# Optimization experiments

Hardware: AMD Instinct MI355X
Metric: run time of the kernel (lower is better)

Reference implementation:

```python
import jax, jax.numpy as jnp
import numpy as np

B, L, D, H = 32, 512, 512, 8          # batch(=num_nodes), seq len, model_size, num_heads
HD = D // H                            # head size
E_DIM, N_EDGES, N_PATHS = 128, 4096, 1024  # edge_dim (hardcoded 128), edge table, #(src,dst) pairs
MAXD = H                               # max_path_distance == num_heads


def setup_inputs() -> dict:
    rng = jax.random.key(0)
    ks = jax.random.split(rng, 16)
    n = lambda k, s: jax.random.normal(k, s, jnp.float32)
    idx = jnp.arange(N_PATHS)
    inp = {
        'query': n(ks[0], (B, L, D)),
        'key':   n(ks[1], (B, L, D)),
        'value': n(ks[2], (B, L, D)),
        'mask':  jnp.ones((B, 1, 1, L), jnp.float32),
        'edge_attr': n(ks[3], (N_EDGES, E_DIM)),
        'path_src': (idx // B).astype(jnp.int32),   # all (src,dst) node pairs
        'path_dst': (idx % B).astype(jnp.int32),
        'path_edges': jax.random.randint(ks[4], (N_PATHS, MAXD), 0, N_EDGES),
        'path_lens': jax.random.randint(ks[5], (N_PATHS,), 1, MAXD + 1),
        # learned params
        'WQ': n(ks[6], (D, D)) * 0.02, 'bQ': jnp.zeros((D,), jnp.float32),
        'WK': n(ks[7], (D, D)) * 0.02, 'bK': jnp.zeros((D,), jnp.float32),
        'WV': n(ks[8], (D, D)) * 0.02, 'bV': jnp.zeros((D,), jnp.float32),
        'WO': n(ks[9], (D, D)) * 0.02, 'bO': jnp.zeros((D,), jnp.float32),
        'edge_vector': n(ks[10], (MAXD, E_DIM)) * 0.05,  # EdgeEncoding weight
        'b_vec': n(ks[11], (MAXD,)) * 0.05,              # SpatialEncoding weight
        'b_scale': jnp.float32(0.001),
        'c_scale': jnp.float32(0.001),
    }
    return inp


def reference(query, key, value, mask, edge_attr, path_src, path_dst, path_edges,
              path_lens, WQ, bQ, WK, bK, WV, bV, WO, bO, edge_vector, b_vec,
              b_scale, c_scale):
    def split_heads(x):  # [B,L,D] -> [B,H,L,HD]
        return x.reshape(B, L, H, HD).transpose(0, 2, 1, 3)

    q = split_heads(jnp.einsum('bld,de->ble', query, WQ) + bQ)
    k = split_heads(jnp.einsum('bld,de->ble', key, WK) + bK)
    v = split_heads(jnp.einsum('bld,de->ble', value, WV) + bV)

    score = jnp.einsum('bhqd,bhkd->bhqk', q, k) / jnp.sqrt(jnp.float32(HD))

    pl = jnp.minimum(path_lens, MAXD).astype(jnp.int32)  # clipped path lengths

    # SpatialEncoding: spatial[src,dst] = b_vec[min(len,maxd)-1]
    spatial = jnp.zeros((B, B), jnp.float32).at[path_src, path_dst].set(b_vec[pl - 1])
    b_mean = spatial.mean(axis=1)  # [B]

    # EdgeEncoding: cij[src,dst] = mean_k <edge_vector[k], edge_attr[path[k]]>
    pe = edge_attr[path_edges]                       # [P,MAXD,E]  batched gather
    dots = jnp.einsum('ke,pke->pk', edge_vector, pe)  # [P,MAXD]
    kmask = (jnp.arange(MAXD)[None, :] < pl[:, None]).astype(jnp.float32)
    cvals = jnp.where(pl > 0, (dots * kmask).sum(1) / jnp.maximum(pl, 1), 0.0)
    cij = jnp.zeros((B, B), jnp.float32).at[path_src, path_dst].set(cvals)
    c_mean = cij.mean(axis=1)  # [B]

    bias = (b_scale * b_mean + c_scale * c_mean)[:, None, None, None]
    score = score + bias + (1.0 - mask) * (-1e9)

    alpha = jax.nn.softmax(score, axis=-1)
    ctx = jnp.einsum('bhqk,bhkd->bhqd', alpha, v)
    ctx = ctx.transpose(0, 2, 1, 3).reshape(B, L, D)
    return jnp.einsum('bld,de->ble', ctx, WO) + bO
```

## Files before the change

kernel.cpp:

```cpp
#include <hip/hip_runtime.h>
#include <hip/hip_bf16.h>

#define B_  32
#define L_  512
#define D_  512
#define H_  8
#define HD_ 64

typedef __attribute__((ext_vector_type(8))) short bf16x8;
typedef __attribute__((ext_vector_type(4))) short bf16x4;
typedef __attribute__((ext_vector_type(4))) float f32x4;

__device__ __forceinline__ short f2bf(float f) {
  union { float f; unsigned u; } x; x.f = f;
  unsigned r = x.u + 0x7FFFu + ((x.u >> 16) & 1u);
  return (short)(r >> 16);
}

__device__ __forceinline__ void gll16(const void* g, void* l) {
  __builtin_amdgcn_global_load_lds(
      (const __attribute__((address_space(1))) unsigned int*)g,
      (__attribute__((address_space(3))) unsigned int*)l, 16, 0, 0);
}

__device__ __forceinline__ bf16x8 cvt8(f32x4 a, f32x4 b) {
  union { __hip_bfloat162 h[4]; bf16x8 v; } u;
  u.h[0] = __float22bfloat162_rn(float2{a[0], a[1]});
  u.h[1] = __float22bfloat162_rn(float2{a[2], a[3]});
  u.h[2] = __float22bfloat162_rn(float2{b[0], b[1]});
  u.h[3] = __float22bfloat162_rn(float2{b[2], b[3]});
  return u.v;
}

#define DS_FENCE() do { asm volatile("s_waitcnt lgkmcnt(0)" ::: "memory"); \
                        __builtin_amdgcn_sched_barrier(0); } while (0)

__global__ __launch_bounds__(256) void wt_kernel(
    const float* __restrict__ WQ, const float* __restrict__ WK,
    const float* __restrict__ WV, const float* __restrict__ WO,
    short* __restrict__ wt) {
  __shared__ float tile[32][33];
  int wz = blockIdx.z;
  const float* W = (wz == 0) ? WQ : (wz == 1) ? WK : (wz == 2) ? WV : WO;
  int k0 = blockIdx.y * 32, n0 = blockIdx.x * 32;
  int tr = threadIdx.x >> 5, tc = threadIdx.x & 31;
#pragma unroll
  for (int i = 0; i < 4; ++i)
    tile[tr + i * 8][tc] = W[(size_t)(k0 + tr + i * 8) * D_ + n0 + tc];
  __syncthreads();
#pragma unroll
  for (int i = 0; i < 4; ++i)
    wt[((size_t)wz * D_ + n0 + tr + i * 8) * D_ + k0 + tc] =
        f2bf(tile[tc][tr + i * 8]);
}

__global__ __launch_bounds__(256, 3) void gemm_qkv(
    const float* __restrict__ Xq, const float* __restrict__ Xk,
    const float* __restrict__ Xv, const short* __restrict__ wt,
    const float* __restrict__ bQ, const float* __restrict__ bK,
    const float* __restrict__ bV,
    short* __restrict__ q_ws, short* __restrict__ k_ws,
    short* __restrict__ vt_ws) {
  __shared__ __align__(16) char lds[49152];
  char* Al = lds;
  char* Bl = lds + 16384;

  int mode = blockIdx.z;
  const float* A = (mode == 0) ? Xq : (mode == 1) ? Xk : Xv;
  const short* WT = wt + (size_t)mode * D_ * D_;
  const float* bias = (mode == 0) ? bQ : (mode == 1) ? bK : bV;

  int wgid = blockIdx.x + 2 * blockIdx.y;
  int xcd = wgid & 7, idx = wgid >> 3;
  int m0 = (xcd * 32 + (idx >> 1)) * 64;
  int n0 = (idx & 1) * 256;

  int tid = threadIdx.x, lane = tid & 63, w = tid >> 6;
  int wr = w >> 1, wc = w & 1, g = lane >> 4, lr = lane & 15;

  f32x4 acc[2][8] = {};

#pragma unroll
  for (int ks = 0; ks < 8; ++ks) {
    __syncthreads();
#pragma unroll
    for (int j = 0; j < 4; ++j) {
      int e = w * 4 + j;
      int row = e * 4 + (lane >> 4);
      int chunk = (lane & 15) ^ (row & 15);
      gll16(A + (size_t)(m0 + row) * D_ + ks * 64 + chunk * 4, Al + e * 1024);
    }
#pragma unroll
    for (int j = 0; j < 8; ++j) {
      int e = w * 8 + j;
      int row = e * 8 + (lane >> 3);
      int chunk = (lane & 7) ^ (lane >> 3);
      gll16(WT + (size_t)(n0 + row) * D_ + ks * 64 + chunk * 8, Bl + e * 1024);
    }
    __syncthreads();
#pragma unroll
    for (int kk = 0; kk < 2; ++kk) {
      bf16x8 af[2], bf_[8];
#pragma unroll
      for (int i = 0; i < 2; ++i) {
        int row = wr * 32 + i * 16 + lr;
        int o0 = ((kk * 8 + g * 2) ^ lr) << 4;
        int o1 = ((kk * 8 + g * 2 + 1) ^ lr) << 4;
        f32x4 lo = *(const f32x4*)(Al + row * 256 + o0);
        f32x4 hi = *(const f32x4*)(Al + row * 256 + o1);
        af[i] = cvt8(lo, hi);
      }
#pragma unroll
      for (int i = 0; i < 8; ++i) {
        int row = wc * 128 + i * 16 + lr;
        bf_[i] = *(const bf16x8*)(Bl + row * 128 +
                                  (((kk * 4 + g) ^ (lr & 7)) << 4));
      }
#pragma unroll
      for (int mi = 0; mi < 2; ++mi)
#pragma unroll
        for (int nj = 0; nj < 8; ++nj)
          acc[mi][nj] = __builtin_amdgcn_mfma_f32_16x16x32_bf16(
              af[mi], bf_[nj], acc[mi][nj], 0, 0, 0);
    }
  }

#pragma unroll
  for (int mi = 0; mi < 2; ++mi) {
#pragma unroll
    for (int nj = 0; nj < 8; ++nj) {
      int n = n0 + wc * 128 + nj * 16 + lr;
      float bb = bias[n];
      int h = n >> 6, hd = n & 63;
#pragma unroll
      for (int rr = 0; rr < 4; ++rr) {
        int m = m0 + wr * 32 + mi * 16 + g * 4 + rr;
        int b = m >> 9, l = m & 511;
        short v = f2bf(acc[mi][nj][rr] + bb);
        if (mode == 0)
          q_ws[(((size_t)b * H_ + h) * L_ + l) * HD_ + hd] = v;
        else if (mode == 1)
          k_ws[(((size_t)b * H_ + h) * L_ + l) * HD_ + hd] = v;
        else
          vt_ws[(((size_t)b * H_ + h) * HD_ + hd) * L_ + l] = v;
      }
    }
  }
}

__global__ __launch_bounds__(256, 4) void attn_kernel(
    const short* __restrict__ q_ws, const short* __restrict__ k_ws,
    const short* __restrict__ vt_ws, const float* __restrict__ mask,
    short* __restrict__ ctx_ws) {
  __shared__ __align__(16) char lds[40960];
  int wg = blockIdx.x;
  int bh   = (wg & 7) * 32 + (wg >> 6);
  int qblk = (wg >> 3) & 7;
  int b = bh >> 3, h = bh & 7;
  int tid = threadIdx.x, lane = tid & 63, w = tid >> 6;
  int g = lane >> 4, lr = lane & 15;
  char* Pl = lds + 32768 + w * 2048;
  int qbase = qblk * 64 + w * 16;

  const short* Qh  = q_ws  + (size_t)bh * (L_ * HD_);
  const short* Kh  = k_ws  + (size_t)bh * (L_ * HD_);
  const short* VTh = vt_ws + (size_t)bh * (HD_ * L_);
  const float* mrow = mask + (size_t)b * L_;

  bf16x8 aq0 = *(const bf16x8*)(Qh + (size_t)(qbase + lr) * HD_ + g * 8);
  bf16x8 aq1 = *(const bf16x8*)(Qh + (size_t)(qbase + lr) * HD_ + 32 + g * 8);

  float mb_all[32];
#pragma unroll
  for (int ch = 0; ch < 8; ++ch)
#pragma unroll
    for (int kt = 0; kt < 4; ++kt)
      mb_all[ch * 4 + kt] = (1.0f - mrow[ch * 64 + kt * 16 + lr]) * -1e9f;

  int rowin = lane >> 3;
  int sch8 = ((lane & 7) ^ rowin) * 8;

#pragma unroll
  for (int j = 0; j < 2; ++j) {
    int e = w * 2 + j, row = e * 8 + rowin;
    gll16(Kh + (size_t)row * HD_ + sch8, lds + e * 1024);
    gll16(VTh + (size_t)row * L_ + sch8, lds + 16384 + e * 1024);
  }
  __syncthreads();

  f32x4 c[4] = {};
  float m[4] = {-1e30f, -1e30f, -1e30f, -1e30f};
  float sum[4] = {0.f, 0.f, 0.f, 0.f};

#pragma unroll
  for (int ch = 0; ch < 8; ++ch) {
    const char* Kb = lds + (ch & 1) * 8192;
    const char* Vb = lds + 16384 + (ch & 1) * 8192;
    if (ch < 7) {
      char* Kn = lds + ((ch + 1) & 1) * 8192;
      char* Vn = lds + 16384 + ((ch + 1) & 1) * 8192;
#pragma unroll
      for (int j = 0; j < 2; ++j) {
        int e = w * 2 + j, row = e * 8 + rowin;
        gll16(Kh + ((size_t)(ch + 1) * 64 + row) * HD_ + sch8, Kn + e * 1024);
        gll16(VTh + (size_t)row * L_ + (ch + 1) * 64 + sch8, Vn + e * 1024);
      }
    }

    f32x4 s[4];
    __builtin_amdgcn_s_setprio(1);
#pragma unroll
    for (int kt = 0; kt < 4; ++kt) {
      int row = kt * 16 + lr;
      bf16x8 bk0 = *(const bf16x8*)(Kb + row * 128 + ((g ^ (lr & 7)) << 4));
      bf16x8 bk1 = *(const bf16x8*)(Kb + row * 128 + (((4 + g) ^ (lr & 7)) << 4));
      f32x4 a = {0.f, 0.f, 0.f, 0.f};
      a = __builtin_amdgcn_mfma_f32_16x16x32_bf16(aq0, bk0, a, 0, 0, 0);
      a = __builtin_amdgcn_mfma_f32_16x16x32_bf16(aq1, bk1, a, 0, 0, 0);
#pragma unroll
      for (int rr = 0; rr < 4; ++rr)
        a[rr] = a[rr] * 0.125f + mb_all[ch * 4 + kt];
      s[kt] = a;
    }
    __builtin_amdgcn_s_setprio(0);

    float pmax[4];
#pragma unroll
    for (int rr = 0; rr < 4; ++rr)
      pmax[rr] = fmaxf(fmaxf(s[0][rr], s[1][rr]), fmaxf(s[2][rr], s[3][rr]));
#pragma unroll
    for (int off = 1; off < 16; off <<= 1)
#pragma unroll
      for (int rr = 0; rr < 4; ++rr)
        pmax[rr] = fmaxf(pmax[rr], __shfl_xor(pmax[rr], off, 64));

    int ok = (pmax[0] - m[0] <= 8.f) & (pmax[1] - m[1] <= 8.f) &
             (pmax[2] - m[2] <= 8.f) & (pmax[3] - m[3] <= 8.f);
    if (!__all(ok)) {
      float scl[4];
#pragma unroll
      for (int rr = 0; rr < 4; ++rr) {
        float mn = fmaxf(m[rr], pmax[rr]);
        scl[rr] = __expf(m[rr] - mn);
        m[rr] = mn;
        sum[rr] *= scl[rr];
      }
#pragma unroll
      for (int nt = 0; nt < 4; ++nt)
#pragma unroll
        for (int rr = 0; rr < 4; ++rr) c[nt][rr] *= scl[rr];
    }

#pragma unroll
    for (int kt = 0; kt < 4; ++kt) {
      int col2 = (kt * 16 + lr) * 2;
#pragma unroll
      for (int rr = 0; rr < 4; ++rr) {
        float p = __expf(s[kt][rr] - m[rr]);
        sum[rr] += p;
        int row = g * 4 + rr;
        *(short*)(Pl + row * 128 + (col2 ^ ((row & 7) << 4))) = f2bf(p);
      }
    }
    DS_FENCE();

    __builtin_amdgcn_s_setprio(1);
#pragma unroll
    for (int kk = 0; kk < 2; ++kk) {
      bf16x8 ap = *(const bf16x8*)(Pl + lr * 128 +
                                   (((kk * 4 + g) ^ (lr & 7)) << 4));
#pragma unroll
      for (int nt = 0; nt < 4; ++nt) {
        int row = nt * 16 + lr;
        bf16x8 bv = *(const bf16x8*)(Vb + row * 128 +
                                     (((kk * 4 + g) ^ (lr & 7)) << 4));
        c[nt] = __builtin_amdgcn_mfma_f32_16x16x32_bf16(ap, bv, c[nt], 0, 0, 0);
      }
    }
    __builtin_amdgcn_s_setprio(0);
    DS_FENCE();
    if (ch < 7) __syncthreads();
  }

  float inv[4];
#pragma unroll
  for (int off = 1; off < 16; off <<= 1)
#pragma unroll
    for (int rr = 0; rr < 4; ++rr) sum[rr] += __shfl_xor(sum[rr], off, 64);
#pragma unroll
  for (int rr = 0; rr < 4; ++rr) inv[rr] = 1.0f / sum[rr];

#pragma unroll
  for (int nt = 0; nt < 4; ++nt) {
    int hd = nt * 16 + lr;
#pragma unroll
    for (int rr = 0; rr < 4; ++rr) {
      int qrow = qbase + g * 4 + rr;
      ctx_ws[(((size_t)b * L_ + qrow) * H_ + h) * HD_ + hd] =
          f2bf(c[nt][rr] * inv[rr]);
    }
  }
}

__global__ __launch_bounds__(256, 4) void gemm_out(
    const short* __restrict__ ctx, const short* __restrict__ wt3,
    const float* __restrict__ bO, float* __restrict__ out) {
  __shared__ __align__(16) char lds[24576];
  char* Al = lds;
  char* Bl = lds + 8192;
  int wgid = blockIdx.x + 4 * blockIdx.y;
  int xcd = wgid & 7, idx = wgid >> 3;
  int m0 = (xcd * 32 + (idx >> 2)) * 64;
  int n0 = (idx & 3) * 128;
  int tid = threadIdx.x, lane = tid & 63, w = tid >> 6;
  int wr = w >> 1, wc = w & 1, g = lane >> 4, lr = lane & 15;

  f32x4 acc[2][4] = {};

#pragma unroll
  for (int ks = 0; ks < 8; ++ks) {
    __syncthreads();
#pragma unroll
    for (int j = 0; j < 2; ++j) {
      int e = w * 2 + j;
      int row = e * 8 + (lane >> 3);
      int chunk = (lane & 7) ^ (lane >> 3);
      gll16(ctx + (size_t)(m0 + row) * D_ + ks * 64 + chunk * 8, Al + e * 1024);
    }
#pragma unroll
    for (int j = 0; j < 4; ++j) {
      int e = w * 4 + j;
      int row = e * 8 + (lane >> 3);
      int chunk = (lane & 7) ^ (lane >> 3);
      gll16(wt3 + (size_t)(n0 + row) * D_ + ks * 64 + chunk * 8, Bl + e * 1024);
    }
    __syncthreads();
#pragma unroll
    for (int kk = 0; kk < 2; ++kk) {
      bf16x8 af[2], bf_[4];
#pragma unroll
      for (int i = 0; i < 2; ++i) {
        int row = wr * 32 + i * 16 + lr;
        af[i] = *(const bf16x8*)(Al + row * 128 +
                                 (((kk * 4 + g) ^ (lr & 7)) << 4));
      }
#pragma unroll
      for (int i = 0; i < 4; ++i) {
        int row = wc * 64 + i * 16 + lr;
        bf_[i] = *(const bf16x8*)(Bl + row * 128 +
                                  (((kk * 4 + g) ^ (lr & 7)) << 4));
      }
#pragma unroll
      for (int mi = 0; mi < 2; ++mi)
#pragma unroll
        for (int nj = 0; nj < 4; ++nj)
          acc[mi][nj] = __builtin_amdgcn_mfma_f32_16x16x32_bf16(
              af[mi], bf_[nj], acc[mi][nj], 0, 0, 0);
    }
  }
#pragma unroll
  for (int mi = 0; mi < 2; ++mi) {
#pragma unroll
    for (int nj = 0; nj < 4; ++nj) {
      int n = n0 + wc * 64 + nj * 16 + lr;
      float bb = bO[n];
#pragma unroll
      for (int rr = 0; rr < 4; ++rr) {
        int m = m0 + wr * 32 + mi * 16 + g * 4 + rr;
        out[(size_t)m * D_ + n] = acc[mi][nj][rr] + bb;
      }
    }
  }
}

extern "C" void kernel_launch(void* const* d_in, const int* in_sizes, int n_in,
                              void* d_out, int out_size, void* d_ws,
                              size_t ws_size, hipStream_t stream) {
  const float* query = (const float*)d_in[0];
  const float* key   = (const float*)d_in[1];
  const float* value = (const float*)d_in[2];
  const float* mask  = (const float*)d_in[3];
  const float* WQ = (const float*)d_in[9];
  const float* bQ = (const float*)d_in[10];
  const float* WK = (const float*)d_in[11];
  const float* bK = (const float*)d_in[12];
  const float* WV = (const float*)d_in[13];
  const float* bV = (const float*)d_in[14];
  const float* WO = (const float*)d_in[15];
  const float* bO = (const float*)d_in[16];

  short* ws  = (short*)d_ws;
  short* wt  = ws;
  short* q   = ws + 1048576;
  short* k   = q + 8388608;
  short* vt  = k + 8388608;
  short* ctx = vt + 8388608;
  float* out = (float*)d_out;

  wt_kernel<<<dim3(16, 16, 4), 256, 0, stream>>>(WQ, WK, WV, WO, wt);
  gemm_qkv<<<dim3(2, 256, 3), 256, 0, stream>>>(query, key, value, wt,
                                                bQ, bK, bV, q, k, vt);
  attn_kernel<<<2048, 256, 0, stream>>>(q, k, vt, mask, ctx);
  gemm_out<<<dim3(4, 256), 256, 0, stream>>>(ctx, wt + 3 * 262144, bO, out);
}
```

Before: 129.1 us.

## Halve QKV GEMM k-tile for higher occupancy and use exp2 softmax

```diff
diff --git a/kernel.cpp b/kernel.cpp
--- a/kernel.cpp
+++ b/kernel.cpp
@@ -6,6 +6,7 @@
 #define D_  512
 #define H_  8
 #define HD_ 64
+#define LOG2E 1.44269504f
 
 typedef __attribute__((ext_vector_type(8))) short bf16x8;
 typedef __attribute__((ext_vector_type(4))) short bf16x4;
@@ -54,16 +55,16 @@
         f2bf(tile[tc][tr + i * 8]);
 }
 
-__global__ __launch_bounds__(256, 3) void gemm_qkv(
+__global__ __launch_bounds__(256, 4) void gemm_qkv(
     const float* __restrict__ Xq, const float* __restrict__ Xk,
     const float* __restrict__ Xv, const short* __restrict__ wt,
     const float* __restrict__ bQ, const float* __restrict__ bK,
     const float* __restrict__ bV,
     short* __restrict__ q_ws, short* __restrict__ k_ws,
     short* __restrict__ vt_ws) {
-  __shared__ __align__(16) char lds[49152];
+  __shared__ __align__(16) char lds[24576];
   char* Al = lds;
-  char* Bl = lds + 16384;
+  char* Bl = lds + 8192;
 
   int mode = blockIdx.z;
   const float* A = (mode == 0) ? Xq : (mode == 1) ? Xk : Xv;
@@ -81,48 +82,47 @@
   f32x4 acc[2][8] = {};
 
 #pragma unroll
-  for (int ks = 0; ks < 8; ++ks) {
+  for (int ks = 0; ks < 16; ++ks) {
     __syncthreads();
+#pragma unroll
+    for (int j = 0; j < 2; ++j) {
+      int e = w * 2 + j;
+      int row = e * 8 + (lane >> 3);
+      int chunk = (lane & 7) ^ (lane >> 3);
+      gll16(A + (size_t)(m0 + row) * D_ + ks * 32 + chunk * 4, Al + e * 1024);
+    }
 #pragma unroll
     for (int j = 0; j < 4; ++j) {
       int e = w * 4 + j;
-      int row = e * 4 + (lane >> 4);
-      int chunk = (lane & 15) ^ (row & 15);
-      gll16(A + (size_t)(m0 + row) * D_ + ks * 64 + chunk * 4, Al + e * 1024);
-    }
-#pragma unroll
-    for (int j = 0; j < 8; ++j) {
-      int e = w * 8 + j;
-      int row = e * 8 + (lane >> 3);
-      int chunk = (lane & 7) ^ (lane >> 3);
-      gll16(WT + (size_t)(n0 + row) * D_ + ks * 64 + chunk * 8, Bl + e * 1024);
+      int rowp = e * 8 + (lane >> 3);
+      int raw = (lane & 7) ^ (lane >> 3);
+      int n = n0 + rowp * 2 + (raw >> 2);
+      gll16(WT + (size_t)n * D_ + ks * 32 + (raw & 3) * 8, Bl + e * 1024);
     }
     __syncthreads();
-#pragma unroll
-    for (int kk = 0; kk < 2; ++kk) {
-      bf16x8 af[2], bf_[8];
-#pragma unroll
-      for (int i = 0; i < 2; ++i) {
-        int row = wr * 32 + i * 16 + lr;
-        int o0 = ((kk * 8 + g * 2) ^ lr) << 4;
-        int o1 = ((kk * 8 + g * 2 + 1) ^ lr) << 4;
-        f32x4 lo = *(const f32x4*)(Al + row * 256 + o0);
-        f32x4 hi = *(const f32x4*)(Al + row * 256 + o1);
-        af[i] = cvt8(lo, hi);
-      }
-#pragma unroll
-      for (int i = 0; i < 8; ++i) {
-        int row = wc * 128 + i * 16 + lr;
-        bf_[i] = *(const bf16x8*)(Bl + row * 128 +
-                                  (((kk * 4 + g) ^ (lr & 7)) << 4));
-      }
-#pragma unroll
-      for (int mi = 0; mi < 2; ++mi)
-#pragma unroll
-        for (int nj = 0; nj < 8; ++nj)
-          acc[mi][nj] = __builtin_amdgcn_mfma_f32_16x16x32_bf16(
-              af[mi], bf_[nj], acc[mi][nj], 0, 0, 0);
-    }
+    bf16x8 af[2], bf_[8];
+#pragma unroll
+    for (int i = 0; i < 2; ++i) {
+      int row = wr * 32 + i * 16 + lr;
+      int o0 = ((2 * g) ^ (lr & 7)) << 4;
+      int o1 = ((2 * g + 1) ^ (lr & 7)) << 4;
+      f32x4 lo = *(const f32x4*)(Al + row * 128 + o0);
+      f32x4 hi = *(const f32x4*)(Al + row * 128 + o1);
+      af[i] = cvt8(lo, hi);
+    }
+#pragma unroll
+    for (int i = 0; i < 8; ++i) {
+      int n = wc * 128 + i * 16 + lr;
+      int rowp = n >> 1;
+      int slot8 = (((n & 1) << 2) + g) ^ (rowp & 7);
+      bf_[i] = *(const bf16x8*)(Bl + rowp * 128 + slot8 * 16);
+    }
+#pragma unroll
+    for (int mi = 0; mi < 2; ++mi)
+#pragma unroll
+      for (int nj = 0; nj < 8; ++nj)
+        acc[mi][nj] = __builtin_amdgcn_mfma_f32_16x16x32_bf16(
+            af[mi], bf_[nj], acc[mi][nj], 0, 0, 0);
   }
 
 #pragma unroll
@@ -175,7 +175,8 @@
   for (int ch = 0; ch < 8; ++ch)
 #pragma unroll
     for (int kt = 0; kt < 4; ++kt)
-      mb_all[ch * 4 + kt] = (1.0f - mrow[ch * 64 + kt * 16 + lr]) * -1e9f;
+      mb_all[ch * 4 + kt] =
+          (1.0f - mrow[ch * 64 + kt * 16 + lr]) * (-1e9f * LOG2E);
 
   int rowin = lane >> 3;
   int sch8 = ((lane & 7) ^ rowin) * 8;
@@ -219,7 +220,7 @@
       a = __builtin_amdgcn_mfma_f32_16x16x32_bf16(aq1, bk1, a, 0, 0, 0);
 #pragma unroll
       for (int rr = 0; rr < 4; ++rr)
-        a[rr] = a[rr] * 0.125f + mb_all[ch * 4 + kt];
+        a[rr] = a[rr] * (0.125f * LOG2E) + mb_all[ch * 4 + kt];
       s[kt] = a;
     }
     __builtin_amdgcn_s_setprio(0);
@@ -234,14 +235,14 @@
       for (int rr = 0; rr < 4; ++rr)
         pmax[rr] = fmaxf(pmax[rr], __shfl_xor(pmax[rr], off, 64));
 
-    int ok = (pmax[0] - m[0] <= 8.f) & (pmax[1] - m[1] <= 8.f) &
-             (pmax[2] - m[2] <= 8.f) & (pmax[3] - m[3] <= 8.f);
+    int ok = (pmax[0] - m[0] <= 8.f * LOG2E) & (pmax[1] - m[1] <= 8.f * LOG2E) &
+             (pmax[2] - m[2] <= 8.f * LOG2E) & (pmax[3] - m[3] <= 8.f * LOG2E);
     if (!__all(ok)) {
       float scl[4];
 #pragma unroll
       for (int rr = 0; rr < 4; ++rr) {
         float mn = fmaxf(m[rr], pmax[rr]);
-        scl[rr] = __expf(m[rr] - mn);
+        scl[rr] = exp2f(m[rr] - mn);
         m[rr] = mn;
         sum[rr] *= scl[rr];
       }
@@ -254,13 +255,19 @@
 #pragma unroll
     for (int kt = 0; kt < 4; ++kt) {
       int col2 = (kt * 16 + lr) * 2;
-#pragma unroll
-      for (int rr = 0; rr < 4; ++rr) {
-        float p = __expf(s[kt][rr] - m[rr]);
-        sum[rr] += p;
-        int row = g * 4 + rr;
-        *(short*)(Pl + row * 128 + (col2 ^ ((row & 7) << 4))) = f2bf(p);
-      }
+      float p0 = exp2f(s[kt][0] - m[0]);
+      float p1 = exp2f(s[kt][1] - m[1]);
+      float p2 = exp2f(s[kt][2] - m[2]);
+      float p3 = exp2f(s[kt][3] - m[3]);
+      sum[0] += p0; sum[1] += p1; sum[2] += p2; sum[3] += p3;
+      union { __hip_bfloat162 h; short s2[2]; } a01, a23;
+      a01.h = __float22bfloat162_rn(float2{p0, p1});
+      a23.h = __float22bfloat162_rn(float2{p2, p3});
+      int r0 = g * 4;
+      *(short*)(Pl + (r0 + 0) * 128 + (col2 ^ (((r0 + 0) & 7) << 4))) = a01.s2[0];
+      *(short*)(Pl + (r0 + 1) * 128 + (col2 ^ (((r0 + 1) & 7) << 4))) = a01.s2[1];
+      *(short*)(Pl + (r0 + 2) * 128 + (col2 ^ (((r0 + 2) & 7) << 4))) = a23.s2[0];
+      *(short*)(Pl + (r0 + 3) * 128 + (col2 ^ (((r0 + 3) & 7) << 4))) = a23.s2[1];
     }
     DS_FENCE();
 
```

After: 147.0 us. 1.14x slower.
